# Kernel tuning notes

Hardware: AMD Instinct MI355X
Metric: run time of the kernel (lower is better)

Reference implementation:

```python
import jax, jax.numpy as jnp
import numpy as np

N = 100000
E = 1600000
R = 4
D_IN = 128
D_H = 128
C = 2


def _rgcn_conv(x, W, src, dst, et):
    """PyG RGCNConv, root_weight=False, bias=False, aggr='mean'.
    x: [N, d_in], W: [R, d_in, d_out]. Per relation: mean over incoming
    edges of that relation of (x[src] @ W_r), summed over relations.
    """
    n, r = x.shape[0], W.shape[0]
    xw = jnp.einsum('ni,rio->rno', x, W)          # [R, N, d_out]
    m = xw[et, src]                               # [E, d_out] per-edge messages
    key = dst * r + et                            # segment per (dst, relation)
    sums = jax.ops.segment_sum(m, key, num_segments=n * r)
    cnt = jax.ops.segment_sum(jnp.ones((m.shape[0],), m.dtype), key, num_segments=n * r)
    mean = sums / jnp.maximum(cnt, 1.0)[:, None]  # [N*R, d_out]
    return mean.reshape(n, r, -1).sum(axis=1)     # sum over relations -> [N, d_out]


def setup_inputs() -> dict:
    key = jax.random.key(0)
    k = jax.random.split(key, 6)
    x = jax.random.normal(k[0], (N, D_IN), dtype=jnp.float32)
    edge_index = jax.random.randint(k[1], (2, E), 0, N, dtype=jnp.int32)
    edge_type = jax.random.randint(k[2], (E,), 0, R, dtype=jnp.int32)
    # Glorot-ish scaled relation weights per layer
    W1 = jax.random.normal(k[3], (R, D_IN, D_H), dtype=jnp.float32) / np.sqrt(D_IN)
    W2 = jax.random.normal(k[4], (R, D_H, D_H), dtype=jnp.float32) / np.sqrt(D_H)
    W3 = jax.random.normal(k[5], (R, D_H, C), dtype=jnp.float32) / np.sqrt(D_H)
    return {"x": x, "edge_index": edge_index, "edge_type": edge_type,
            "W1": W1, "W2": W2, "W3": W3}


def reference(x, edge_index, edge_type, W1, W2, W3):
    src, dst = edge_index[0], edge_index[1]
    # eval mode: dropout is identity
    h = _rgcn_conv(x, W1, src, dst, edge_type)
    h = jnp.tanh(h)
    h = _rgcn_conv(h, W2, src, dst, edge_type)
    h = jnp.tanh(h)
    h = _rgcn_conv(h, W3, src, dst, edge_type)   # [N, C] logits
    return jax.nn.softmax(h, axis=1), h
```

## Files before the change

kernel.cpp:

```cpp
#include <hip/hip_runtime.h>
#include <math.h>

#define N_NODES 100000
#define N_EDGES 1600000
#define RREL 4
#define DDIM 128
#define KDIM 512
#define NKEY 400000

typedef __bf16 bf16x8 __attribute__((ext_vector_type(8)));
typedef float f32x4 __attribute__((ext_vector_type(4)));

__device__ __forceinline__ float bflo(unsigned u){ return __builtin_bit_cast(float, u << 16); }
__device__ __forceinline__ float bfhi(unsigned u){ return __builtin_bit_cast(float, u & 0xffff0000u); }
__device__ __forceinline__ unsigned f2bf(float f){
  unsigned u = __builtin_bit_cast(unsigned, f);
  return (u + 0x7fffu + ((u >> 16) & 1u)) >> 16;
}
__device__ __forceinline__ int iclamp(int v, int lo, int hi){
  return v < lo ? lo : (v > hi ? hi : v);
}


__global__ void hist_kernel(const int* __restrict__ dst, const int* __restrict__ et,
                            int* __restrict__ counts){
  int e = blockIdx.x * 256 + threadIdx.x;
  int key = iclamp(dst[e] * RREL + et[e], 0, NKEY - 1);
  atomicAdd(&counts[key], 1);
}

__global__ void scan_local(const int* __restrict__ in, int* __restrict__ out,
                           int* __restrict__ bsums, int K){
  __shared__ int s[1024];
  int t = threadIdx.x;
  int i = blockIdx.x * 1024 + t;
  int v = (i < K) ? in[i] : 0;
  s[t] = v; __syncthreads();
  for (int off = 1; off < 1024; off <<= 1){
    int x = (t >= off) ? s[t - off] : 0;
    __syncthreads();
    s[t] += x;
    __syncthreads();
  }
  if (i < K) out[i] = s[t] - v;
  if (t == 1023) bsums[blockIdx.x] = s[t];
}

__global__ void scan_sums(int* __restrict__ b, int nb){
  __shared__ int s[1024];
  int t = threadIdx.x;
  int v = (t < nb) ? b[t] : 0;
  s[t] = v; __syncthreads();
  for (int off = 1; off < 1024; off <<= 1){
    int x = (t >= off) ? s[t - off] : 0;
    __syncthreads();
    s[t] += x;
    __syncthreads();
  }
  if (t < nb) b[t] = s[t] - v;
}

__global__ void scan_add(int* __restrict__ out, int* __restrict__ cursor,
                         const int* __restrict__ bsums, int K, int total){
  int t = threadIdx.x;
  int i = blockIdx.x * 1024 + t;
  if (i < K){
    int v = out[i] + bsums[blockIdx.x];
    out[i] = v;
    cursor[i] = v;
  }
  if (i == 0) out[K] = total;
}

__global__ void scatter_kernel(const int* __restrict__ src, const int* __restrict__ dst,
                               const int* __restrict__ et, int* __restrict__ cursor,
                               int* __restrict__ ssrc){
  int e = blockIdx.x * 256 + threadIdx.x;
  int key = iclamp(dst[e] * RREL + et[e], 0, NKEY - 1);
  int p = atomicAdd(&cursor[key], 1);
  p = iclamp(p, 0, N_EDGES - 1);
  ssrc[p] = iclamp(src[e], 0, N_NODES - 1);
}


__global__ void convert_x(const float* __restrict__ x, unsigned* __restrict__ xb){
  int i = blockIdx.x * 256 + threadIdx.x;
  float2 v = *(const float2*)(x + (size_t)i * 2);
  xb[i] = f2bf(v.x) | (f2bf(v.y) << 16);
}


__global__ void transpose_w(const float* __restrict__ W, unsigned short* __restrict__ Bt){
  int idx = blockIdx.x * 256 + threadIdx.x;
  int k = idx >> 7, n = idx & 127;
  Bt[n * KDIM + k] = (unsigned short)f2bf(W[idx]);
}


__global__ __launch_bounds__(256) void fused_layer(const unsigned* __restrict__ hin,
                                                   const int* __restrict__ ssrc,
                                                   const int* __restrict__ offs,
                                                   const __bf16* __restrict__ Bt,
                                                   unsigned short* __restrict__ hout){
  int tid = threadIdx.x;
  int w = tid >> 6, lane = tid & 63;
  int l15 = lane & 15, quad = lane >> 4;
  int n0w = blockIdx.x * 64 + w * 16;
  int n = n0w + l15;
  int valid = (n < N_NODES);

  f32x4 accC[8];
  #pragma unroll
  for (int tc = 0; tc < 8; tc++) accC[tc] = (f32x4){0.f, 0.f, 0.f, 0.f};

  #pragma unroll
  for (int r = 0; r < RREL; r++){
    int ob = valid ? (n * 4 + r) : 0;
    int beg = iclamp(offs[ob], 0, N_EDGES);
    int end = iclamp(offs[ob + 1], beg, N_EDGES);
    if (!valid){ beg = 0; end = 0; }

    float ac[32];
    #pragma unroll
    for (int j = 0; j < 32; j++) ac[j] = 0.f;

    int i = beg;
    int nxt = (i < end) ? ssrc[i] : 0;
    while (i < end){
      int cur = iclamp(nxt, 0, N_NODES - 1);
      i++;
      nxt = (i < end) ? ssrc[i] : 0;
      const uint4* row = (const uint4*)(hin + (size_t)cur * 64 + quad * 4);
      uint4 u0 = row[0];
      uint4 u1 = row[4];
      uint4 u2 = row[8];
      uint4 u3 = row[12];
      ac[ 0] += bflo(u0.x); ac[ 1] += bfhi(u0.x); ac[ 2] += bflo(u0.y); ac[ 3] += bfhi(u0.y);
      ac[ 4] += bflo(u0.z); ac[ 5] += bfhi(u0.z); ac[ 6] += bflo(u0.w); ac[ 7] += bfhi(u0.w);
      ac[ 8] += bflo(u1.x); ac[ 9] += bfhi(u1.x); ac[10] += bflo(u1.y); ac[11] += bfhi(u1.y);
      ac[12] += bflo(u1.z); ac[13] += bfhi(u1.z); ac[14] += bflo(u1.w); ac[15] += bfhi(u1.w);
      ac[16] += bflo(u2.x); ac[17] += bfhi(u2.x); ac[18] += bflo(u2.y); ac[19] += bfhi(u2.y);
      ac[20] += bflo(u2.z); ac[21] += bfhi(u2.z); ac[22] += bflo(u2.w); ac[23] += bfhi(u2.w);
      ac[24] += bflo(u3.x); ac[25] += bfhi(u3.x); ac[26] += bflo(u3.y); ac[27] += bfhi(u3.y);
      ac[28] += bflo(u3.z); ac[29] += bfhi(u3.z); ac[30] += bflo(u3.w); ac[31] += bfhi(u3.w);
    }
    int cnt = end - beg;
    float sc = (cnt > 0) ? 1.0f / (float)cnt : 0.0f;

    #pragma unroll
    for (int s = 0; s < 4; s++){
      uint4 pv;
      pv.x = f2bf(ac[s * 8 + 0] * sc) | (f2bf(ac[s * 8 + 1] * sc) << 16);
      pv.y = f2bf(ac[s * 8 + 2] * sc) | (f2bf(ac[s * 8 + 3] * sc) << 16);
      pv.z = f2bf(ac[s * 8 + 4] * sc) | (f2bf(ac[s * 8 + 5] * sc) << 16);
      pv.w = f2bf(ac[s * 8 + 6] * sc) | (f2bf(ac[s * 8 + 7] * sc) << 16);
      bf16x8 af = __builtin_bit_cast(bf16x8, pv);
      const __bf16* bbase = Bt + r * 128 + s * 32 + quad * 8;
      #pragma unroll
      for (int tc = 0; tc < 8; tc++){
        bf16x8 bfr = *(const bf16x8*)(bbase + (size_t)(tc * 16 + l15) * KDIM);
        accC[tc] = __builtin_amdgcn_mfma_f32_16x16x32_bf16(af, bfr, accC[tc], 0, 0, 0);
      }
    }
  }

  #pragma unroll
  for (int tc = 0; tc < 8; tc++){
    #pragma unroll
    for (int reg = 0; reg < 4; reg++){
      int n2 = n0w + quad * 4 + reg;
      if (n2 < N_NODES){
        float v = tanhf(accC[tc][reg]);
        hout[(size_t)n2 * 128 + tc * 16 + l15] = (unsigned short)f2bf(v);
      }
    }
  }
}


__global__ void fused_head(const unsigned* __restrict__ h2,
                           const int* __restrict__ ssrc,
                           const int* __restrict__ offs,
                           const float* __restrict__ W3f,
                           float* __restrict__ out){
  int n = blockIdx.x * 4 + (threadIdx.x >> 6);
  int lane = threadIdx.x & 63;
  float dA = 0.f, dB = 0.f;
  int ob = n * 4;
  #pragma unroll
  for (int r = 0; r < RREL; r++){
    int beg = iclamp(offs[ob + r], 0, N_EDGES);
    int end = iclamp(offs[ob + r + 1], beg, N_EDGES);
    float a0=0.f,a1=0.f,b0=0.f,b1=0.f,c0=0.f,c1=0.f,d0=0.f,d1=0.f;
    int i = beg;
    for (; i + 4 <= end; i += 4){
      int s0 = iclamp(ssrc[i],     0, N_NODES-1);
      int s1 = iclamp(ssrc[i + 1], 0, N_NODES-1);
      int s2 = iclamp(ssrc[i + 2], 0, N_NODES-1);
      int s3 = iclamp(ssrc[i + 3], 0, N_NODES-1);
      unsigned u0 = h2[(size_t)s0 * 64 + lane];
      unsigned u1 = h2[(size_t)s1 * 64 + lane];
      unsigned u2 = h2[(size_t)s2 * 64 + lane];
      unsigned u3 = h2[(size_t)s3 * 64 + lane];
      a0 += bflo(u0); a1 += bfhi(u0);
      b0 += bflo(u1); b1 += bfhi(u1);
      c0 += bflo(u2); c1 += bfhi(u2);
      d0 += bflo(u3); d1 += bfhi(u3);
    }
    for (; i < end; i++){
      unsigned u = h2[(size_t)iclamp(ssrc[i], 0, N_NODES-1) * 64 + lane];
      a0 += bflo(u); a1 += bfhi(u);
    }
    int cnt = end - beg;
    float sc = (cnt > 0) ? 1.0f / (float)cnt : 0.0f;
    float m0 = (a0 + b0 + c0 + d0) * sc, m1 = (a1 + b1 + c1 + d1) * sc;
    float4 wv = *(const float4*)(W3f + r * 256 + lane * 4);
    dA += m0 * wv.x + m1 * wv.z;
    dB += m0 * wv.y + m1 * wv.w;
  }
  #pragma unroll
  for (int m = 32; m >= 1; m >>= 1){
    dA += __shfl_xor(dA, m);
    dB += __shfl_xor(dB, m);
  }
  if (lane == 0){
    float mx = fmaxf(dA, dB);
    float e0 = __expf(dA - mx), e1 = __expf(dB - mx);
    float inv = 1.0f / (e0 + e1);
    *(float2*)(out + 2 * n) = (float2){e0 * inv, e1 * inv};
    *(float2*)(out + 2 * N_NODES + 2 * n) = (float2){dA, dB};
  }
}


extern "C" void kernel_launch(void* const* d_in, const int* in_sizes, int n_in,
                              void* d_out, int out_size, void* d_ws, size_t ws_size,
                              hipStream_t stream){
  const float* x  = (const float*)d_in[0];
  const int* ei   = (const int*)d_in[1];
  const int* et   = (const int*)d_in[2];
  const float* W1 = (const float*)d_in[3];
  const float* W2 = (const float*)d_in[4];
  const float* W3 = (const float*)d_in[5];
  float* out = (float*)d_out;
  const int* src = ei;
  const int* dst = ei + N_EDGES;

  char* p = (char*)d_ws;
  auto alloc = [&](size_t bytes) -> char* {
    char* q = p; p += (bytes + 63) & ~(size_t)63; return q;
  };
  int* counts = (int*)alloc((size_t)NKEY * 4);
  int* cursor = counts;
  int* offs   = (int*)alloc((size_t)(NKEY + 1) * 4);
  int* bsums  = (int*)alloc(1024 * 4);
  int* ssrc   = (int*)alloc((size_t)N_EDGES * 4);
  unsigned short* Bt = (unsigned short*)alloc((size_t)DDIM * KDIM * 2);
  unsigned short* h1 = (unsigned short*)alloc((size_t)N_NODES * DDIM * 2);
  unsigned short* h2 = (unsigned short*)alloc((size_t)N_NODES * DDIM * 2);
  unsigned* xb = (unsigned*)h2;

  hipMemsetAsync(counts, 0, (size_t)NKEY * 4, stream);
  hist_kernel<<<N_EDGES / 256, 256, 0, stream>>>(dst, et, counts);
  int nb = (NKEY + 1023) / 1024;
  scan_local<<<nb, 1024, 0, stream>>>(counts, offs, bsums, NKEY);
  scan_sums<<<1, 1024, 0, stream>>>(bsums, nb);
  scan_add<<<nb, 1024, 0, stream>>>(offs, cursor, bsums, NKEY, N_EDGES);
  scatter_kernel<<<N_EDGES / 256, 256, 0, stream>>>(src, dst, et, cursor, ssrc);

  int fgrid = (N_NODES + 63) / 64;

  convert_x<<<(N_NODES * 64) / 256, 256, 0, stream>>>(x, xb);
  transpose_w<<<(DDIM * KDIM) / 256, 256, 0, stream>>>(W1, Bt);
  fused_layer<<<fgrid, 256, 0, stream>>>(xb, ssrc, offs, (const __bf16*)Bt, h1);
  transpose_w<<<(DDIM * KDIM) / 256, 256, 0, stream>>>(W2, Bt);
  fused_layer<<<fgrid, 256, 0, stream>>>((const unsigned*)h1, ssrc, offs, (const __bf16*)Bt, h2);
  fused_head<<<N_NODES / 4, 256, 0, stream>>>((const unsigned*)h2, ssrc, offs, W3, out);
}
```

Before: 817.3 us.

## Project layer-3 features through W3 before aggregation to shrink gathered data

```diff
diff --git a/kernel.cpp b/kernel.cpp
--- a/kernel.cpp
+++ b/kernel.cpp
@@ -178,52 +178,69 @@
 }
 
 
-__global__ void fused_head(const unsigned* __restrict__ h2,
-                           const int* __restrict__ ssrc,
-                           const int* __restrict__ offs,
-                           const float* __restrict__ W3f,
-                           float* __restrict__ out){
+__global__ void compute_z(const unsigned* __restrict__ h2, const float* __restrict__ W3f,
+                          float* __restrict__ zt){
   int n = blockIdx.x * 4 + (threadIdx.x >> 6);
   int lane = threadIdx.x & 63;
-  float dA = 0.f, dB = 0.f;
-  int ob = n * 4;
+  unsigned u = h2[(size_t)n * 64 + lane];
+  float a = bflo(u), b = bfhi(u);
+  float p[8];
   #pragma unroll
   for (int r = 0; r < RREL; r++){
-    int beg = iclamp(offs[ob + r], 0, N_EDGES);
-    int end = iclamp(offs[ob + r + 1], beg, N_EDGES);
-    float a0=0.f,a1=0.f,b0=0.f,b1=0.f,c0=0.f,c1=0.f,d0=0.f,d1=0.f;
-    int i = beg;
-    for (; i + 4 <= end; i += 4){
-      int s0 = iclamp(ssrc[i],     0, N_NODES-1);
-      int s1 = iclamp(ssrc[i + 1], 0, N_NODES-1);
-      int s2 = iclamp(ssrc[i + 2], 0, N_NODES-1);
-      int s3 = iclamp(ssrc[i + 3], 0, N_NODES-1);
-      unsigned u0 = h2[(size_t)s0 * 64 + lane];
-      unsigned u1 = h2[(size_t)s1 * 64 + lane];
-      unsigned u2 = h2[(size_t)s2 * 64 + lane];
-      unsigned u3 = h2[(size_t)s3 * 64 + lane];
-      a0 += bflo(u0); a1 += bfhi(u0);
-      b0 += bflo(u1); b1 += bfhi(u1);
-      c0 += bflo(u2); c1 += bfhi(u2);
-      d0 += bflo(u3); d1 += bfhi(u3);
-    }
-    for (; i < end; i++){
-      unsigned u = h2[(size_t)iclamp(ssrc[i], 0, N_NODES-1) * 64 + lane];
-      a0 += bflo(u); a1 += bfhi(u);
-    }
-    int cnt = end - beg;
-    float sc = (cnt > 0) ? 1.0f / (float)cnt : 0.0f;
-    float m0 = (a0 + b0 + c0 + d0) * sc, m1 = (a1 + b1 + c1 + d1) * sc;
     float4 wv = *(const float4*)(W3f + r * 256 + lane * 4);
-    dA += m0 * wv.x + m1 * wv.z;
-    dB += m0 * wv.y + m1 * wv.w;
+    p[r * 2]     = a * wv.x + b * wv.z;
+    p[r * 2 + 1] = a * wv.y + b * wv.w;
   }
   #pragma unroll
   for (int m = 32; m >= 1; m >>= 1){
-    dA += __shfl_xor(dA, m);
-    dB += __shfl_xor(dB, m);
+    #pragma unroll
+    for (int j = 0; j < 8; j++) p[j] += __shfl_xor(p[j], m);
   }
   if (lane == 0){
+    *(float4*)(zt + (size_t)n * 8)     = (float4){p[0], p[1], p[2], p[3]};
+    *(float4*)(zt + (size_t)n * 8 + 4) = (float4){p[4], p[5], p[6], p[7]};
+  }
+}
+
+
+__global__ void fused_head2(const float* __restrict__ zt,
+                            const int* __restrict__ ssrc,
+                            const int* __restrict__ offs,
+                            float* __restrict__ out){
+  int k = blockIdx.x * 256 + threadIdx.x;
+  if (k >= NKEY) return;
+  int r = k & 3;
+  int beg = iclamp(offs[k], 0, N_EDGES);
+  int end = iclamp(offs[k + 1], beg, N_EDGES);
+  float a0 = 0.f, a1 = 0.f, b0 = 0.f, b1 = 0.f, c0 = 0.f, c1 = 0.f, d0 = 0.f, d1 = 0.f;
+  int i = beg;
+  for (; i + 4 <= end; i += 4){
+    int s0 = iclamp(ssrc[i],     0, N_NODES - 1);
+    int s1 = iclamp(ssrc[i + 1], 0, N_NODES - 1);
+    int s2 = iclamp(ssrc[i + 2], 0, N_NODES - 1);
+    int s3 = iclamp(ssrc[i + 3], 0, N_NODES - 1);
+    float2 v0 = *(const float2*)(zt + (size_t)s0 * 8 + r * 2);
+    float2 v1 = *(const float2*)(zt + (size_t)s1 * 8 + r * 2);
+    float2 v2 = *(const float2*)(zt + (size_t)s2 * 8 + r * 2);
+    float2 v3 = *(const float2*)(zt + (size_t)s3 * 8 + r * 2);
+    a0 += v0.x; a1 += v0.y;
+    b0 += v1.x; b1 += v1.y;
+    c0 += v2.x; c1 += v2.y;
+    d0 += v3.x; d1 += v3.y;
+  }
+  for (; i < end; i++){
+    int s = iclamp(ssrc[i], 0, N_NODES - 1);
+    float2 v = *(const float2*)(zt + (size_t)s * 8 + r * 2);
+    a0 += v.x; a1 += v.y;
+  }
+  int cnt = end - beg;
+  float sc = (cnt > 0) ? 1.0f / (float)cnt : 0.0f;
+  float dA = (a0 + b0 + c0 + d0) * sc;
+  float dB = (a1 + b1 + c1 + d1) * sc;
+  dA += __shfl_xor(dA, 1); dB += __shfl_xor(dB, 1);
+  dA += __shfl_xor(dA, 2); dB += __shfl_xor(dB, 2);
+  if (r == 0){
+    int n = k >> 2;
     float mx = fmaxf(dA, dB);
     float e0 = __expf(dA - mx), e1 = __expf(dB - mx);
     float inv = 1.0f / (e0 + e1);
@@ -259,6 +276,7 @@
   unsigned short* h1 = (unsigned short*)alloc((size_t)N_NODES * DDIM * 2);
   unsigned short* h2 = (unsigned short*)alloc((size_t)N_NODES * DDIM * 2);
   unsigned* xb = (unsigned*)h2;
+  float* zt = (float*)h1;
 
   hipMemsetAsync(counts, 0, (size_t)NKEY * 4, stream);
   hist_kernel<<<N_EDGES / 256, 256, 0, stream>>>(dst, et, counts);
@@ -275,5 +293,6 @@
   fused_layer<<<fgrid, 256, 0, stream>>>(xb, ssrc, offs, (const __bf16*)Bt, h1);
   transpose_w<<<(DDIM * KDIM) / 256, 256, 0, stream>>>(W2, Bt);
   fused_layer<<<fgrid, 256, 0, stream>>>((const unsigned*)h1, ssrc, offs, (const __bf16*)Bt, h2);
-  fused_head<<<N_NODES / 4, 256, 0, stream>>>((const unsigned*)h2, ssrc, offs, W3, out);
-}
+  compute_z<<<N_NODES / 4, 256, 0, stream>>>((const unsigned*)h2, W3, zt);
+  fused_head2<<<(NKEY + 255) / 256, 256, 0, stream>>>(zt, ssrc, offs, out);
+}
```

Measured after the change: 753.9 us. 1.08x faster.
